# Kernel optimization log

Measured on AMD Instinct MI355X. Metric: run time of the kernel, lower is better.

## Reference

```python
import jax, jax.numpy as jnp
import numpy as np

T, N, C, H, W = 16, 16, 64, 64, 64
V_THRESHOLD = 1.0


def setup_inputs() -> dict:
    key = jax.random.key(0)
    k1, _ = jax.random.split(key)
    x_seq = jax.random.normal(k1, (T, N, C, H, W), dtype=jnp.float32)
    # decay = 1 - alpha = 1 - 1/tau with tau=2.0
    decay = jnp.array([0.5], dtype=jnp.float32)
    return {"x_seq": x_seq, "decay": decay}


def reference(x_seq, decay):
    # Leaky-integrate with hard zero reset at threshold, scanned over T.
    d = decay[0]

    def step(v, x):
        v = v * d + x                      # leak + integrate
        v = jnp.where(v >= V_THRESHOLD, jnp.zeros_like(v), v)  # zero reset
        return v, v

    v0 = jnp.zeros(x_seq.shape[1:], dtype=x_seq.dtype)
    _, v_seq = jax.lax.scan(step, v0, x_seq)
    return v_seq  # [T, N, C, H, W] membrane potentials
```

## Files before the change

### kernel.cpp

```cpp
#include <hip/hip_runtime.h>


#define T_STEPS 16
#define V_THRESHOLD 1.0f

typedef float f32x4 __attribute__((ext_vector_type(4)));

__device__ __forceinline__ void plif_step4(f32x4& v, const f32x4 xv, const float d) {
    v.x = fmaf(v.x, d, xv.x); if (v.x >= V_THRESHOLD) v.x = 0.f;
    v.y = fmaf(v.y, d, xv.y); if (v.y >= V_THRESHOLD) v.y = 0.f;
    v.z = fmaf(v.z, d, xv.z); if (v.z >= V_THRESHOLD) v.z = 0.f;
    v.w = fmaf(v.w, d, xv.w); if (v.w >= V_THRESHOLD) v.w = 0.f;
}

__global__ __launch_bounds__(256) void plif_kernel(
    const f32x4* __restrict__ x,
    const float* __restrict__ decay,
    f32x4*       __restrict__ out,
    long long    stride4)
{
    const long long base =
        ((long long)blockIdx.x * blockDim.x + threadIdx.x) * 2;
    if (base >= stride4) return;
    const float d = decay[0];

    f32x4 va = (f32x4)0.f, vb = (f32x4)0.f;
    long long off = base;

    f32x4 xa = x[off];
    f32x4 xb = x[off + 1];

#pragma unroll
    for (int t = 0; t < T_STEPS; ++t) {
        f32x4 na, nb;
        if (t + 1 < T_STEPS) {
            na = x[off + stride4];
            nb = x[off + stride4 + 1];
        } else {
            na = xa; nb = xb;
        }

        plif_step4(va, xa, d);
        plif_step4(vb, xb, d);

        __builtin_nontemporal_store(va, &out[off]);
        __builtin_nontemporal_store(vb, &out[off + 1]);

        xa = na; xb = nb;
        off += stride4;
    }
}

extern "C" void kernel_launch(void* const* d_in, const int* in_sizes, int n_in,
                              void* d_out, int out_size, void* d_ws, size_t ws_size,
                              hipStream_t stream) {
    const float* x     = (const float*)d_in[0];
    const float* decay = (const float*)d_in[1];
    float* out         = (float*)d_out;

    const long long total   = in_sizes[0];
    const long long spatial = total / T_STEPS;
    const long long stride4 = spatial / 4;

    const int block = 256;
    const long long threads = (stride4 + 1) / 2;
    const int grid  = (int)((threads + block - 1) / block);

    plif_kernel<<<grid, block, 0, stream>>>(
        (const f32x4*)x, decay, (f32x4*)out, stride4);
}
```

Before: 462.4 us.

## Issue all timestep loads upfront with one float4 column per thread

Each thread now handles a single float4 column instead of two. It loads all 16 timesteps into registers before computing, and a sched_barrier stops the compiler from interleaving those loads with the compute. The aim is to raise memory-level parallelism by putting every load in flight at once instead of software-pipelining one step ahead. The cost is about 64 VGPRs for the buffered inputs, and the grid becomes twice as large.

```diff
diff --git a/kernel.cpp b/kernel.cpp
--- a/kernel.cpp
+++ b/kernel.cpp
@@ -6,47 +6,33 @@
 
 typedef float f32x4 __attribute__((ext_vector_type(4)));
 
-__device__ __forceinline__ void plif_step4(f32x4& v, const f32x4 xv, const float d) {
-    v.x = fmaf(v.x, d, xv.x); if (v.x >= V_THRESHOLD) v.x = 0.f;
-    v.y = fmaf(v.y, d, xv.y); if (v.y >= V_THRESHOLD) v.y = 0.f;
-    v.z = fmaf(v.z, d, xv.z); if (v.z >= V_THRESHOLD) v.z = 0.f;
-    v.w = fmaf(v.w, d, xv.w); if (v.w >= V_THRESHOLD) v.w = 0.f;
-}
-
 __global__ __launch_bounds__(256) void plif_kernel(
     const f32x4* __restrict__ x,
     const float* __restrict__ decay,
     f32x4*       __restrict__ out,
     long long    stride4)
 {
-    const long long base =
-        ((long long)blockIdx.x * blockDim.x + threadIdx.x) * 2;
-    if (base >= stride4) return;
+    const long long col = (long long)blockIdx.x * blockDim.x + threadIdx.x;
+    if (col >= stride4) return;
     const float d = decay[0];
 
-    f32x4 va = (f32x4)0.f, vb = (f32x4)0.f;
-    long long off = base;
+    f32x4 xs[T_STEPS];
+#pragma unroll
+    for (int t = 0; t < T_STEPS; ++t)
+        xs[t] = x[col + (long long)t * stride4];
 
-    f32x4 xa = x[off];
-    f32x4 xb = x[off + 1];
+    __builtin_amdgcn_sched_barrier(0);
 
+    f32x4 v = (f32x4)0.f;
+    long long off = col;
 #pragma unroll
     for (int t = 0; t < T_STEPS; ++t) {
-        f32x4 na, nb;
-        if (t + 1 < T_STEPS) {
-            na = x[off + stride4];
-            nb = x[off + stride4 + 1];
-        } else {
-            na = xa; nb = xb;
-        }
-
-        plif_step4(va, xa, d);
-        plif_step4(vb, xb, d);
-
-        __builtin_nontemporal_store(va, &out[off]);
-        __builtin_nontemporal_store(vb, &out[off + 1]);
-
-        xa = na; xb = nb;
+        const f32x4 xv = xs[t];
+        v.x = fmaf(v.x, d, xv.x); if (v.x >= V_THRESHOLD) v.x = 0.f;
+        v.y = fmaf(v.y, d, xv.y); if (v.y >= V_THRESHOLD) v.y = 0.f;
+        v.z = fmaf(v.z, d, xv.z); if (v.z >= V_THRESHOLD) v.z = 0.f;
+        v.w = fmaf(v.w, d, xv.w); if (v.w >= V_THRESHOLD) v.w = 0.f;
+        __builtin_nontemporal_store(v, &out[off]);
         off += stride4;
     }
 }
@@ -63,8 +49,7 @@
     const long long stride4 = spatial / 4;
 
     const int block = 256;
-    const long long threads = (stride4 + 1) / 2;
-    const int grid  = (int)((threads + block - 1) / block);
+    const int grid  = (int)((stride4 + block - 1) / block);
 
     plif_kernel<<<grid, block, 0, stream>>>(
         (const f32x4*)x, decay, (f32x4*)out, stride4);
```

New measurement: 468.7 us. No clear change (+1.4%).
